# Kernel tuning notes

Hardware: AMD Instinct MI355X
Metric: run time of the kernel (lower is better)

Reference implementation:

```python
import jax, jax.numpy as jnp
import numpy as np

TS = 1.0  # simulation time step (Ts from network.yaml)


def alpha_psp(x, tau):
    """SLAYER psp: causal temporal conv of x (time-major, (T,...)) with the
    SRM alpha kernel eps[k] = (k*Ts/tau)*exp(1 - k*Ts/tau), scaled by Ts.
    eps[k] = (Ts*e/tau) * k * d**k with d = exp(-Ts/tau), realized exactly by a
    2-state linear recurrence instead of an O(T^2) FIR."""
    d = jnp.asarray(np.exp(-TS / tau), x.dtype)
    c = jnp.asarray(np.e * TS / tau * TS, x.dtype)  # kernel amp * Ts integration

    def step(carry, x_t):
        u, v = carry                       # u = sum x_s d^(t-1-s); v = sum x_s (t-1-s) d^(t-1-s)
        v_new = d * (v + u)                # -> sum_{s<=t} x_s (t-s) d^(t-s)  (x_t weight 0)
        u_new = d * u + x_t
        return (u_new, v_new), c * v_new

    z = jnp.zeros_like(x[0])
    _, out = jax.lax.scan(step, (z, z), x)
    return out


def lif_spike(u_in, theta, tauRef, scaleRef):
    """SLAYER spike function: sequential threshold over time with alpha-shaped
    refractory response nu[k] = -scaleRef*theta*(k*Ts/tauRef)*exp(1-k*Ts/tauRef)
    added after every spike. Same 2-state recurrence generates the refractory
    sum exactly. u_in is time-major (T, ...). Spike amplitude is 1/Ts."""
    d = jnp.asarray(np.exp(-TS / tauRef), u_in.dtype)
    c = jnp.asarray(-scaleRef * theta * np.e * TS / tauRef, u_in.dtype)

    def step(carry, u_t):
        u, v = carry
        v_new = d * (v + u)                # refractory state from past spikes only
        m = u_t + c * v_new                # membrane potential incl. refractory
        s = (m >= theta).astype(u_t.dtype)
        return (d * u + s, v_new), (s / TS, m)

    z = jnp.zeros_like(u_in[0])
    _, (spikes, membrane) = jax.lax.scan(step, (z, z), u_in)
    return spikes, membrane


def conv2d_t(x, w, pad):
    """Per-time-step 2D conv (SLAYER conv3d with time-kernel 1, no bias).
    x: (T, N, C, H, W), w: (O, I, kh, kw)."""
    T, N, C, H, W = x.shape
    y = jax.lax.conv_general_dilated(
        x.reshape(T * N, C, H, W), w, (1, 1), [(pad, pad), (pad, pad)],
        dimension_numbers=('NCHW', 'OIHW', 'NCHW'))
    return y.reshape(T, N, -1, H, W)


def setup_inputs() -> dict:
    key = jax.random.key(0)
    k1, k2, k3 = jax.random.split(key, 3)
    # binary event spike train, (N, C, H, W, T)
    spikeInput = (jax.random.uniform(k1, (4, 1, 192, 192, 64)) < 0.2).astype(jnp.float32)
    # SLAYER conv weights (bias=False); scaled up (weightScale~100 in SLAYER)
    W1 = jax.random.normal(k2, (1, 1, 5, 5), jnp.float32) * 10.0
    W2 = jax.random.normal(k3, (1, 1, 3, 3), jnp.float32) * 10.0
    return {"spikeInput": spikeInput, "W1": W1, "W2": W2}


def reference(spikeInput, W1, W2):
    x = jnp.moveaxis(spikeInput, -1, 0)          # (T, N, C, H, W) time-major
    psp1 = alpha_psp(x, tau=1.0)                 # slayer1.psp (tauSr=1)
    s1, _ = lif_spike(conv2d_t(psp1, W1, 2), theta=30.0, tauRef=1.0, scaleRef=1.0)
    psp2 = alpha_psp(s1, tau=2.0)                # slayer2.psp (tauSr=2)
    s2, _ = lif_spike(conv2d_t(psp2, W2, 1), theta=50.0, tauRef=2.0, scaleRef=1.0)
    return jnp.moveaxis(s2, 0, -1)               # back to (N, C, H, W, T)
```

## Files before the change

kernel.cpp:

```cpp
#include <hip/hip_runtime.h>


#define HH   192
#define WW   192
#define NIMG 4
#define TT   64
#define NT   256
#define XW   6
#define XH   12

#define E_D 2.718281828459045
static constexpr float D1  = (float)0.36787944117144233;
static constexpr float CP1 = (float)(E_D);
static constexpr float DR1 = (float)0.36787944117144233;
static constexpr float CR1 = (float)(-30.0 * E_D);
static constexpr float D2  = (float)0.6065306597126334;
static constexpr float CP2 = (float)(E_D * 0.5);
static constexpr float DR2 = (float)0.6065306597126334;
static constexpr float CR2 = (float)(-50.0 * E_D * 0.5);
static constexpr float TH1 = 30.0f;
static constexpr float TH2 = 50.0f;

__global__ __launch_bounds__(NT)
void ka_pack(const float* __restrict__ in, unsigned* __restrict__ bitT) {
    const int gw = blockIdx.x * (NT / 64) + (threadIdx.x >> 6);
    const int ln = threadIdx.x & 63;
    const int xw = gw % XW;
    const int ny = gw / XW;
    const float* src = in + ((size_t)ny * WW + xw * 32) * TT + ln;
    unsigned w = 0u;
#pragma unroll
    for (int x = 0; x < 32; x++) {
        const float v = src[(size_t)x * TT];
        w |= (v != 0.f) ? (1u << x) : 0u;
    }
    bitT[((size_t)ny * XW + xw) * TT + ln] = w;
}

__global__ __launch_bounds__(NT, 1)
void kb_layer1(const unsigned* __restrict__ bitT, const float* __restrict__ w1g,
               unsigned short* __restrict__ s1h) {
    __shared__ float lutA[1024];
    __shared__ float lutB[1024];
    __shared__ float lutC[32];
    __shared__ float ct[NT * 65];
    __shared__ uint2 tb[NT];

    const int n = blockIdx.z, ty = blockIdx.y, tx = blockIdx.x;
    const int y0 = ty * 16, x0 = tx * 16;
    const int tid = threadIdx.x;
    const int wv = tid >> 6, ln = tid & 63;

    for (int e = tid; e < 1024; e += NT) {
        float l0 = 0.f, l1 = 0.f, l2 = 0.f, l3 = 0.f;
#pragma unroll
        for (int j = 0; j < 5; j++) {
            if ((e >> j) & 1)       { l0 += w1g[j];     l2 += w1g[10 + j]; }
            if ((e >> (5 + j)) & 1) { l1 += w1g[5 + j]; l3 += w1g[15 + j]; }
        }
        lutA[e] = l0 + l1;
        lutB[e] = l2 + l3;
    }
    if (tid < 32) {
        float s = 0.f;
#pragma unroll
        for (int j = 0; j < 5; j++)
            if ((tid >> j) & 1) s += w1g[20 + j];
        lutC[tid] = s;
    }

    const int a = (x0 - 2) >> 5;
    const int s = (x0 - 2) & 31;
    unsigned w20[8];
#pragma unroll
    for (int rr = 0; rr < 8; rr++) {
        const int gy = y0 - 2 + wv * 4 + rr;
        unsigned wa = 0u, wb = 0u;
        if (gy >= 0 && gy < HH) {
            const unsigned* rp = bitT + ((size_t)(n * HH + gy) * XW) * TT + ln;
            if (a >= 0)     wa = rp[(size_t)a * TT];
            if (a + 1 < XW) wb = rp[(size_t)(a + 1) * TT];
        }
        w20[rr] = (wa >> s) | (wb << (32 - s));
    }
    __syncthreads();

#pragma unroll
    for (int rp = 0; rp < 4; rp++) {
        const int row = wv * 4 + rp;
#pragma unroll
        for (int col = 0; col < 16; col++) {
            const unsigned pA = ((w20[rp + 0] >> col) & 31)
                              | (((w20[rp + 1] >> col) & 31) << 5);
            const unsigned pB = ((w20[rp + 2] >> col) & 31)
                              | (((w20[rp + 3] >> col) & 31) << 5);
            const unsigned pC = (w20[rp + 4] >> col) & 31;
            ct[(row * 16 + col) * 65 + ln] = (lutA[pA] + lutB[pB]) + lutC[pC];
        }
    }
    __syncthreads();

    unsigned slo = 0u, shi = 0u;
    {
        const int px = tid;
        float u1 = 0.f, v1 = 0.f, ur = 0.f, vr = 0.f;
#pragma unroll
        for (int tc = 0; tc < TT; tc += 8) {
            float c8[8];
#pragma unroll
            for (int j = 0; j < 8; j++) c8[j] = ct[px * 65 + tc + j];
#pragma unroll
            for (int j = 0; j < 8; j++) {
                v1 = D1 * (v1 + u1);
                const float p = CP1 * v1;
                u1 = D1 * u1 + c8[j];
                vr = DR1 * (vr + ur);
                const float m = p + CR1 * vr;
                const bool sp = (m >= TH1);
                ur = DR1 * ur + (sp ? 1.f : 0.f);
                const unsigned bit = sp ? (1u << ((tc + j) & 31)) : 0u;
                if (tc < 32) slo |= bit;
                else         shi |= bit;
            }
        }
    }
    tb[tid] = make_uint2(slo, shi);
    __syncthreads();

#pragma unroll
    for (int rp = 0; rp < 4; rp++) {
        const int yl = wv * 4 + rp;
        unsigned h = 0u;
#pragma unroll
        for (int x = 0; x < 16; x++) {
            const uint2 b = tb[yl * 16 + x];
            const unsigned w = (ln < 32) ? b.x : b.y;
            h |= ((w >> (ln & 31)) & 1u) << x;
        }
        s1h[((size_t)(n * HH + y0 + yl) * XH + tx) * TT + ln] =
            (unsigned short)h;
    }
}

__global__ __launch_bounds__(NT, 1)
void kc_layer2(const unsigned short* __restrict__ s1h, const float* __restrict__ w2g,
               float* __restrict__ out) {
    __shared__ float lut3[512];
    __shared__ unsigned short ptile[NT * 66];
    __shared__ uint2 tb[NT];

    const int n = blockIdx.z, ty = blockIdx.y, tx = blockIdx.x;
    const int y0 = ty * 16;
    const int tid = threadIdx.x;
    const int wv = tid >> 6, ln = tid & 63;

#pragma unroll
    for (int e = tid; e < 512; e += NT) {
        float l0 = 0.f, l1 = 0.f, l2 = 0.f;
#pragma unroll
        for (int j = 0; j < 3; j++) {
            if ((e >> j) & 1)       l0 += w2g[j];
            if ((e >> (3 + j)) & 1) l1 += w2g[3 + j];
            if ((e >> (6 + j)) & 1) l2 += w2g[6 + j];
        }
        lut3[e] = (l0 + l1) + l2;
    }

    unsigned w18[6];
#pragma unroll
    for (int rr = 0; rr < 6; rr++) {
        const int gy = y0 - 1 + wv * 4 + rr;
        unsigned hm = 0u, h0 = 0u, hp = 0u;
        if (gy >= 0 && gy < HH) {
            const unsigned short* rp = s1h + ((size_t)(n * HH + gy) * XH) * TT + ln;
            if (tx > 0)      hm = rp[(size_t)(tx - 1) * TT];
            h0 = rp[(size_t)tx * TT];
            if (tx + 1 < XH) hp = rp[(size_t)(tx + 1) * TT];
        }
        w18[rr] = (hm >> 15) | (h0 << 1) | ((hp & 1u) << 17);
    }
    __syncthreads();

#pragma unroll
    for (int rp = 0; rp < 4; rp++) {
        const int row = wv * 4 + rp;
#pragma unroll
        for (int col = 0; col < 16; col++) {
            const unsigned pat = ((w18[rp + 0] >> col) & 7)
                               | (((w18[rp + 1] >> col) & 7) << 3)
                               | (((w18[rp + 2] >> col) & 7) << 6);
            ptile[(row * 16 + col) * 66 + ln] = (unsigned short)pat;
        }
    }
    __syncthreads();

    unsigned olo = 0u, ohi = 0u;
    {
        const int px = tid;
        const unsigned* pp = (const unsigned*)(ptile + px * 66);
        float u2 = 0.f, v2 = 0.f, ur2 = 0.f, vr2 = 0.f;
#pragma unroll
        for (int tc = 0; tc < TT; tc += 8) {
            unsigned q[4];
#pragma unroll
            for (int k = 0; k < 4; k++) q[k] = pp[tc / 2 + k];
            float l[8];
#pragma unroll
            for (int k = 0; k < 4; k++) {
                l[2 * k + 0] = lut3[q[k] & 0x1ffu];
                l[2 * k + 1] = lut3[(q[k] >> 16) & 0x1ffu];
            }
#pragma unroll
            for (int j = 0; j < 8; j++) {
                v2 = D2 * (v2 + u2);
                const float p = CP2 * v2;
                u2 = D2 * u2 + l[j];
                vr2 = DR2 * (vr2 + ur2);
                const float m = p + CR2 * vr2;
                const bool sp = (m >= TH2);
                ur2 = DR2 * ur2 + (sp ? 1.f : 0.f);
                const unsigned bit = sp ? (1u << ((tc + j) & 31)) : 0u;
                if (tc < 32) olo |= bit;
                else         ohi |= bit;
            }
        }
    }
    tb[tid] = make_uint2(olo, ohi);
    __syncthreads();

    const int sh = ln & 31;
#pragma unroll
    for (int k = 0; k < 64; k++) {
        const int p = wv * 64 + k;
        const uint2 b = tb[p];
        const unsigned w = (ln < 32) ? b.x : b.y;
        out[((size_t)(n * HH + y0 + (p >> 4)) * WW + tx * 16 + (p & 15)) * TT
            + ln] = (float)((w >> sh) & 1u);
    }
}

extern "C" void kernel_launch(void* const* d_in, const int* in_sizes, int n_in,
                              void* d_out, int out_size, void* d_ws, size_t ws_size,
                              hipStream_t stream) {
    const float* in = (const float*)d_in[0];
    const float* w1 = (const float*)d_in[1];
    const float* w2 = (const float*)d_in[2];
    float* out = (float*)d_out;

    char* ws = (char*)d_ws;
    unsigned*       bitT = (unsigned*)ws;
    unsigned short* s1h  = (unsigned short*)(ws + (2ull << 20));

    const int ka_blocks = (NIMG * HH * XW) / (NT / 64);
    dim3 tgrid(WW / 16, HH / 16, NIMG);
    ka_pack  <<<ka_blocks, NT, 0, stream>>>(in, bitT);
    kb_layer1<<<tgrid, NT, 0, stream>>>(bitT, w1, s1h);
    kc_layer2<<<tgrid, NT, 0, stream>>>(s1h, w2, out);
}
```

Before: 123.7 us.

## Fuse input bit-packing into layer1 kernel and widen blocks to 1024 threads

Removes the separate packing kernel. Layer1 now reads the float input directly and builds 20-bit row masks, including the halo, into shared memory. Both tile kernels move to 1024-thread blocks, with one wave per output row for the pattern and output stages, while only 256 threads run the sequential time recurrence. This saves a launch and the bitT round trip through global memory. In exchange, halo columns are read redundantly from the float input, and most threads sit idle during the serial recurrence.

```diff
diff --git a/kernel.cpp b/kernel.cpp
--- a/kernel.cpp
+++ b/kernel.cpp
@@ -5,8 +5,7 @@
 #define WW   192
 #define NIMG 4
 #define TT   64
-#define NT   256
-#define XW   6
+#define NT   1024
 #define XH   12
 
 #define E_D 2.718281828459045
@@ -21,37 +20,23 @@
 static constexpr float TH1 = 30.0f;
 static constexpr float TH2 = 50.0f;
 
-__global__ __launch_bounds__(NT)
-void ka_pack(const float* __restrict__ in, unsigned* __restrict__ bitT) {
-    const int gw = blockIdx.x * (NT / 64) + (threadIdx.x >> 6);
-    const int ln = threadIdx.x & 63;
-    const int xw = gw % XW;
-    const int ny = gw / XW;
-    const float* src = in + ((size_t)ny * WW + xw * 32) * TT + ln;
-    unsigned w = 0u;
-#pragma unroll
-    for (int x = 0; x < 32; x++) {
-        const float v = src[(size_t)x * TT];
-        w |= (v != 0.f) ? (1u << x) : 0u;
-    }
-    bitT[((size_t)ny * XW + xw) * TT + ln] = w;
-}
-
 __global__ __launch_bounds__(NT, 1)
-void kb_layer1(const unsigned* __restrict__ bitT, const float* __restrict__ w1g,
+void kb_layer1(const float* __restrict__ in, const float* __restrict__ w1g,
                unsigned short* __restrict__ s1h) {
-    __shared__ float lutA[1024];
-    __shared__ float lutB[1024];
-    __shared__ float lutC[32];
-    __shared__ float ct[NT * 65];
-    __shared__ uint2 tb[NT];
+    __shared__ float    lutA[1024];
+    __shared__ float    lutB[1024];
+    __shared__ float    lutC[32];
+    __shared__ unsigned rowT[20 * 64];
+    __shared__ float    ct[256 * 65];
+    __shared__ uint2    tb[256];
 
     const int n = blockIdx.z, ty = blockIdx.y, tx = blockIdx.x;
     const int y0 = ty * 16, x0 = tx * 16;
     const int tid = threadIdx.x;
     const int wv = tid >> 6, ln = tid & 63;
 
-    for (int e = tid; e < 1024; e += NT) {
+    {
+        const int e = tid;
         float l0 = 0.f, l1 = 0.f, l2 = 0.f, l3 = 0.f;
 #pragma unroll
         for (int j = 0; j < 5; j++) {
@@ -69,41 +54,44 @@
         lutC[tid] = s;
     }
 
-    const int a = (x0 - 2) >> 5;
-    const int s = (x0 - 2) & 31;
-    unsigned w20[8];
-#pragma unroll
-    for (int rr = 0; rr < 8; rr++) {
-        const int gy = y0 - 2 + wv * 4 + rr;
-        unsigned wa = 0u, wb = 0u;
+    for (int r = wv; r < 20; r += 16) {
+        const int gy = y0 - 2 + r;
+        unsigned word = 0u;
         if (gy >= 0 && gy < HH) {
-            const unsigned* rp = bitT + ((size_t)(n * HH + gy) * XW) * TT + ln;
-            if (a >= 0)     wa = rp[(size_t)a * TT];
-            if (a + 1 < XW) wb = rp[(size_t)(a + 1) * TT];
-        }
-        w20[rr] = (wa >> s) | (wb << (32 - s));
-    }
-    __syncthreads();
-
-#pragma unroll
-    for (int rp = 0; rp < 4; rp++) {
-        const int row = wv * 4 + rp;
+            const float* rowp = in + ((size_t)(n * HH + gy) * WW) * TT + ln;
+#pragma unroll
+            for (int c = 0; c < 20; c++) {
+                const int gx = x0 - 2 + c;
+                if (gx >= 0 && gx < WW) {
+                    const float v = rowp[(size_t)gx * TT];
+                    word |= (v != 0.f) ? (1u << c) : 0u;
+                }
+            }
+        }
+        rowT[r * 64 + ln] = word;
+    }
+    __syncthreads();
+
+    {
+        unsigned w20[5];
+#pragma unroll
+        for (int dy = 0; dy < 5; dy++) w20[dy] = rowT[(wv + dy) * 64 + ln];
 #pragma unroll
         for (int col = 0; col < 16; col++) {
-            const unsigned pA = ((w20[rp + 0] >> col) & 31)
-                              | (((w20[rp + 1] >> col) & 31) << 5);
-            const unsigned pB = ((w20[rp + 2] >> col) & 31)
-                              | (((w20[rp + 3] >> col) & 31) << 5);
-            const unsigned pC = (w20[rp + 4] >> col) & 31;
-            ct[(row * 16 + col) * 65 + ln] = (lutA[pA] + lutB[pB]) + lutC[pC];
-        }
-    }
-    __syncthreads();
-
-    unsigned slo = 0u, shi = 0u;
-    {
+            const unsigned pA = ((w20[0] >> col) & 31)
+                              | (((w20[1] >> col) & 31) << 5);
+            const unsigned pB = ((w20[2] >> col) & 31)
+                              | (((w20[3] >> col) & 31) << 5);
+            const unsigned pC = (w20[4] >> col) & 31;
+            ct[(wv * 16 + col) * 65 + ln] = (lutA[pA] + lutB[pB]) + lutC[pC];
+        }
+    }
+    __syncthreads();
+
+    if (tid < 256) {
         const int px = tid;
         float u1 = 0.f, v1 = 0.f, ur = 0.f, vr = 0.f;
+        unsigned slo = 0u, shi = 0u;
 #pragma unroll
         for (int tc = 0; tc < TT; tc += 8) {
             float c8[8];
@@ -123,21 +111,19 @@
                 else         shi |= bit;
             }
         }
-    }
-    tb[tid] = make_uint2(slo, shi);
-    __syncthreads();
-
-#pragma unroll
-    for (int rp = 0; rp < 4; rp++) {
-        const int yl = wv * 4 + rp;
+        tb[px] = make_uint2(slo, shi);
+    }
+    __syncthreads();
+
+    {
         unsigned h = 0u;
 #pragma unroll
         for (int x = 0; x < 16; x++) {
-            const uint2 b = tb[yl * 16 + x];
+            const uint2 b = tb[wv * 16 + x];
             const unsigned w = (ln < 32) ? b.x : b.y;
             h |= ((w >> (ln & 31)) & 1u) << x;
         }
-        s1h[((size_t)(n * HH + y0 + yl) * XH + tx) * TT + ln] =
+        s1h[((size_t)(n * HH + y0 + wv) * XH + tx) * TT + ln] =
             (unsigned short)h;
     }
 }
@@ -145,17 +131,18 @@
 __global__ __launch_bounds__(NT, 1)
 void kc_layer2(const unsigned short* __restrict__ s1h, const float* __restrict__ w2g,
                float* __restrict__ out) {
-    __shared__ float lut3[512];
-    __shared__ unsigned short ptile[NT * 66];
-    __shared__ uint2 tb[NT];
+    __shared__ float          lut3[512];
+    __shared__ unsigned       wrow[18 * 64];
+    __shared__ unsigned short ptile[256 * 66];
+    __shared__ uint2          tb[256];
 
     const int n = blockIdx.z, ty = blockIdx.y, tx = blockIdx.x;
     const int y0 = ty * 16;
     const int tid = threadIdx.x;
     const int wv = tid >> 6, ln = tid & 63;
 
-#pragma unroll
-    for (int e = tid; e < 512; e += NT) {
+    if (tid < 512) {
+        const int e = tid;
         float l0 = 0.f, l1 = 0.f, l2 = 0.f;
 #pragma unroll
         for (int j = 0; j < 3; j++) {
@@ -166,39 +153,39 @@
         lut3[e] = (l0 + l1) + l2;
     }
 
-    unsigned w18[6];
-#pragma unroll
-    for (int rr = 0; rr < 6; rr++) {
-        const int gy = y0 - 1 + wv * 4 + rr;
+    for (int r = wv; r < 18; r += 16) {
+        const int gy = y0 - 1 + r;
         unsigned hm = 0u, h0 = 0u, hp = 0u;
         if (gy >= 0 && gy < HH) {
-            const unsigned short* rp = s1h + ((size_t)(n * HH + gy) * XH) * TT + ln;
+            const unsigned short* rp =
+                s1h + ((size_t)(n * HH + gy) * XH) * TT + ln;
             if (tx > 0)      hm = rp[(size_t)(tx - 1) * TT];
             h0 = rp[(size_t)tx * TT];
             if (tx + 1 < XH) hp = rp[(size_t)(tx + 1) * TT];
         }
-        w18[rr] = (hm >> 15) | (h0 << 1) | ((hp & 1u) << 17);
-    }
-    __syncthreads();
-
-#pragma unroll
-    for (int rp = 0; rp < 4; rp++) {
-        const int row = wv * 4 + rp;
+        wrow[r * 64 + ln] = (hm >> 15) | (h0 << 1) | ((hp & 1u) << 17);
+    }
+    __syncthreads();
+
+    {
+        unsigned w18[3];
+#pragma unroll
+        for (int dy = 0; dy < 3; dy++) w18[dy] = wrow[(wv + dy) * 64 + ln];
 #pragma unroll
         for (int col = 0; col < 16; col++) {
-            const unsigned pat = ((w18[rp + 0] >> col) & 7)
-                               | (((w18[rp + 1] >> col) & 7) << 3)
-                               | (((w18[rp + 2] >> col) & 7) << 6);
-            ptile[(row * 16 + col) * 66 + ln] = (unsigned short)pat;
-        }
-    }
-    __syncthreads();
-
-    unsigned olo = 0u, ohi = 0u;
-    {
+            const unsigned pat = ((w18[0] >> col) & 7)
+                               | (((w18[1] >> col) & 7) << 3)
+                               | (((w18[2] >> col) & 7) << 6);
+            ptile[(wv * 16 + col) * 66 + ln] = (unsigned short)pat;
+        }
+    }
+    __syncthreads();
+
+    if (tid < 256) {
         const int px = tid;
         const unsigned* pp = (const unsigned*)(ptile + px * 66);
         float u2 = 0.f, v2 = 0.f, ur2 = 0.f, vr2 = 0.f;
+        unsigned olo = 0u, ohi = 0u;
 #pragma unroll
         for (int tc = 0; tc < TT; tc += 8) {
             unsigned q[4];
@@ -224,18 +211,17 @@
                 else         ohi |= bit;
             }
         }
-    }
-    tb[tid] = make_uint2(olo, ohi);
+        tb[px] = make_uint2(olo, ohi);
+    }
     __syncthreads();
 
     const int sh = ln & 31;
 #pragma unroll
-    for (int k = 0; k < 64; k++) {
-        const int p = wv * 64 + k;
-        const uint2 b = tb[p];
+    for (int k = 0; k < 16; k++) {
+        const uint2 b = tb[wv * 16 + k];
         const unsigned w = (ln < 32) ? b.x : b.y;
-        out[((size_t)(n * HH + y0 + (p >> 4)) * WW + tx * 16 + (p & 15)) * TT
-            + ln] = (float)((w >> sh) & 1u);
+        out[((size_t)(n * HH + y0 + wv) * WW + tx * 16 + k) * TT + ln] =
+            (float)((w >> sh) & 1u);
     }
 }
 
@@ -247,13 +233,9 @@
     const float* w2 = (const float*)d_in[2];
     float* out = (float*)d_out;
 
-    char* ws = (char*)d_ws;
-    unsigned*       bitT = (unsigned*)ws;
-    unsigned short* s1h  = (unsigned short*)(ws + (2ull << 20));
-
-    const int ka_blocks = (NIMG * HH * XW) / (NT / 64);
+    unsigned short* s1h = (unsigned short*)d_ws;
+
     dim3 tgrid(WW / 16, HH / 16, NIMG);
-    ka_pack  <<<ka_blocks, NT, 0, stream>>>(in, bitT);
-    kb_layer1<<<tgrid, NT, 0, stream>>>(bitT, w1, s1h);
+    kb_layer1<<<tgrid, NT, 0, stream>>>(in, w1, s1h);
     kc_layer2<<<tgrid, NT, 0, stream>>>(s1h, w2, out);
 }
```

Result: slower. 148.4 us (+19.9%).

## Shrink conv-scan tiles to 4x16 pixels with one scan wave per block

Applied to the files above, without the earlier changes.

Both layer kernels now process a 4-row by 16-column tile per block instead of 16x16, giving four times as many blocks, and each block's LDS shrinks enough for several to fit per CU. Only the first wave runs the sequential time scan (64 pixels), while all four waves build the conv tile and write outputs. The aim is more blocks and more concurrent waves to hide the latency of the serial scan and of the global loads. The cost is three of four waves idling during the scan, and LUT construction plus halo row loads being repeated across four times as many blocks.

```diff
diff --git a/kernel.cpp b/kernel.cpp
--- a/kernel.cpp
+++ b/kernel.cpp
@@ -37,20 +37,21 @@
     bitT[((size_t)ny * XW + xw) * TT + ln] = w;
 }
 
-__global__ __launch_bounds__(NT, 1)
-void kb_layer1(const unsigned* __restrict__ bitT, const float* __restrict__ w1g,
-               unsigned short* __restrict__ s1h) {
+__global__ __launch_bounds__(NT, 4)
+void l1_convscan(const unsigned* __restrict__ bitT, const float* __restrict__ w1g,
+                 unsigned short* __restrict__ s1h) {
     __shared__ float lutA[1024];
     __shared__ float lutB[1024];
     __shared__ float lutC[32];
-    __shared__ float ct[NT * 65];
-    __shared__ uint2 tb[NT];
-
-    const int n = blockIdx.z, ty = blockIdx.y, tx = blockIdx.x;
-    const int y0 = ty * 16, x0 = tx * 16;
+    __shared__ float ct[64 * 65];
+    __shared__ uint2 tb[64];
+
+    const int n = blockIdx.z, ys = blockIdx.y, xs = blockIdx.x;
+    const int y0 = ys * 4, x0 = xs * 16;
     const int tid = threadIdx.x;
     const int wv = tid >> 6, ln = tid & 63;
 
+#pragma unroll
     for (int e = tid; e < 1024; e += NT) {
         float l0 = 0.f, l1 = 0.f, l2 = 0.f, l3 = 0.f;
 #pragma unroll
@@ -71,39 +72,34 @@
 
     const int a = (x0 - 2) >> 5;
     const int s = (x0 - 2) & 31;
-    unsigned w20[8];
-#pragma unroll
-    for (int rr = 0; rr < 8; rr++) {
-        const int gy = y0 - 2 + wv * 4 + rr;
+    const int gyb = y0 + wv;
+    unsigned w20[5];
+#pragma unroll
+    for (int dy = 0; dy < 5; dy++) {
+        const int gy = gyb - 2 + dy;
         unsigned wa = 0u, wb = 0u;
         if (gy >= 0 && gy < HH) {
             const unsigned* rp = bitT + ((size_t)(n * HH + gy) * XW) * TT + ln;
             if (a >= 0)     wa = rp[(size_t)a * TT];
             if (a + 1 < XW) wb = rp[(size_t)(a + 1) * TT];
         }
-        w20[rr] = (wa >> s) | (wb << (32 - s));
-    }
-    __syncthreads();
-
-#pragma unroll
-    for (int rp = 0; rp < 4; rp++) {
-        const int row = wv * 4 + rp;
-#pragma unroll
-        for (int col = 0; col < 16; col++) {
-            const unsigned pA = ((w20[rp + 0] >> col) & 31)
-                              | (((w20[rp + 1] >> col) & 31) << 5);
-            const unsigned pB = ((w20[rp + 2] >> col) & 31)
-                              | (((w20[rp + 3] >> col) & 31) << 5);
-            const unsigned pC = (w20[rp + 4] >> col) & 31;
-            ct[(row * 16 + col) * 65 + ln] = (lutA[pA] + lutB[pB]) + lutC[pC];
-        }
-    }
-    __syncthreads();
-
-    unsigned slo = 0u, shi = 0u;
-    {
+        w20[dy] = (wa >> s) | (wb << (32 - s));
+    }
+    __syncthreads();
+
+#pragma unroll
+    for (int col = 0; col < 16; col++) {
+        const unsigned pA = ((w20[0] >> col) & 31) | (((w20[1] >> col) & 31) << 5);
+        const unsigned pB = ((w20[2] >> col) & 31) | (((w20[3] >> col) & 31) << 5);
+        const unsigned pC = (w20[4] >> col) & 31;
+        ct[(wv * 16 + col) * 65 + ln] = (lutA[pA] + lutB[pB]) + lutC[pC];
+    }
+    __syncthreads();
+
+    if (tid < 64) {
         const int px = tid;
         float u1 = 0.f, v1 = 0.f, ur = 0.f, vr = 0.f;
+        unsigned slo = 0u, shi = 0u;
 #pragma unroll
         for (int tc = 0; tc < TT; tc += 8) {
             float c8[8];
@@ -123,34 +119,31 @@
                 else         shi |= bit;
             }
         }
-    }
-    tb[tid] = make_uint2(slo, shi);
-    __syncthreads();
-
-#pragma unroll
-    for (int rp = 0; rp < 4; rp++) {
-        const int yl = wv * 4 + rp;
+        tb[px] = make_uint2(slo, shi);
+    }
+    __syncthreads();
+
+    {
         unsigned h = 0u;
 #pragma unroll
         for (int x = 0; x < 16; x++) {
-            const uint2 b = tb[yl * 16 + x];
+            const uint2 b = tb[wv * 16 + x];
             const unsigned w = (ln < 32) ? b.x : b.y;
             h |= ((w >> (ln & 31)) & 1u) << x;
         }
-        s1h[((size_t)(n * HH + y0 + yl) * XH + tx) * TT + ln] =
-            (unsigned short)h;
-    }
-}
-
-__global__ __launch_bounds__(NT, 1)
-void kc_layer2(const unsigned short* __restrict__ s1h, const float* __restrict__ w2g,
-               float* __restrict__ out) {
-    __shared__ float lut3[512];
-    __shared__ unsigned short ptile[NT * 66];
-    __shared__ uint2 tb[NT];
-
-    const int n = blockIdx.z, ty = blockIdx.y, tx = blockIdx.x;
-    const int y0 = ty * 16;
+        s1h[((size_t)(n * HH + gyb) * XH + xs) * TT + ln] = (unsigned short)h;
+    }
+}
+
+__global__ __launch_bounds__(NT, 4)
+void l2_convscan(const unsigned short* __restrict__ s1h, const float* __restrict__ w2g,
+                 float* __restrict__ out) {
+    __shared__ float          lut3[512];
+    __shared__ unsigned short ptile[64 * 66];
+    __shared__ uint2          tb[64];
+
+    const int n = blockIdx.z, ys = blockIdx.y, xs = blockIdx.x;
+    const int y0 = ys * 4;
     const int tid = threadIdx.x;
     const int wv = tid >> 6, ln = tid & 63;
 
@@ -166,39 +159,36 @@
         lut3[e] = (l0 + l1) + l2;
     }
 
-    unsigned w18[6];
-#pragma unroll
-    for (int rr = 0; rr < 6; rr++) {
-        const int gy = y0 - 1 + wv * 4 + rr;
+    const int gyb = y0 + wv;
+    unsigned w18[3];
+#pragma unroll
+    for (int dy = 0; dy < 3; dy++) {
+        const int gy = gyb - 1 + dy;
         unsigned hm = 0u, h0 = 0u, hp = 0u;
         if (gy >= 0 && gy < HH) {
             const unsigned short* rp = s1h + ((size_t)(n * HH + gy) * XH) * TT + ln;
-            if (tx > 0)      hm = rp[(size_t)(tx - 1) * TT];
-            h0 = rp[(size_t)tx * TT];
-            if (tx + 1 < XH) hp = rp[(size_t)(tx + 1) * TT];
-        }
-        w18[rr] = (hm >> 15) | (h0 << 1) | ((hp & 1u) << 17);
-    }
-    __syncthreads();
-
-#pragma unroll
-    for (int rp = 0; rp < 4; rp++) {
-        const int row = wv * 4 + rp;
-#pragma unroll
-        for (int col = 0; col < 16; col++) {
-            const unsigned pat = ((w18[rp + 0] >> col) & 7)
-                               | (((w18[rp + 1] >> col) & 7) << 3)
-                               | (((w18[rp + 2] >> col) & 7) << 6);
-            ptile[(row * 16 + col) * 66 + ln] = (unsigned short)pat;
-        }
-    }
-    __syncthreads();
-
-    unsigned olo = 0u, ohi = 0u;
-    {
+            if (xs > 0)      hm = rp[(size_t)(xs - 1) * TT];
+            h0 = rp[(size_t)xs * TT];
+            if (xs + 1 < XH) hp = rp[(size_t)(xs + 1) * TT];
+        }
+        w18[dy] = (hm >> 15) | (h0 << 1) | ((hp & 1u) << 17);
+    }
+    __syncthreads();
+
+#pragma unroll
+    for (int col = 0; col < 16; col++) {
+        const unsigned pat = ((w18[0] >> col) & 7)
+                           | (((w18[1] >> col) & 7) << 3)
+                           | (((w18[2] >> col) & 7) << 6);
+        ptile[(wv * 16 + col) * 66 + ln] = (unsigned short)pat;
+    }
+    __syncthreads();
+
+    if (tid < 64) {
         const int px = tid;
         const unsigned* pp = (const unsigned*)(ptile + px * 66);
         float u2 = 0.f, v2 = 0.f, ur2 = 0.f, vr2 = 0.f;
+        unsigned olo = 0u, ohi = 0u;
 #pragma unroll
         for (int tc = 0; tc < TT; tc += 8) {
             unsigned q[4];
@@ -224,18 +214,17 @@
                 else         ohi |= bit;
             }
         }
-    }
-    tb[tid] = make_uint2(olo, ohi);
+        tb[px] = make_uint2(olo, ohi);
+    }
     __syncthreads();
 
     const int sh = ln & 31;
 #pragma unroll
-    for (int k = 0; k < 64; k++) {
-        const int p = wv * 64 + k;
-        const uint2 b = tb[p];
+    for (int k = 0; k < 16; k++) {
+        const uint2 b = tb[wv * 16 + k];
         const unsigned w = (ln < 32) ? b.x : b.y;
-        out[((size_t)(n * HH + y0 + (p >> 4)) * WW + tx * 16 + (p & 15)) * TT
-            + ln] = (float)((w >> sh) & 1u);
+        out[((size_t)(n * HH + gyb) * WW + xs * 16 + k) * TT + ln] =
+            (float)((w >> sh) & 1u);
     }
 }
 
@@ -252,8 +241,8 @@
     unsigned short* s1h  = (unsigned short*)(ws + (2ull << 20));
 
     const int ka_blocks = (NIMG * HH * XW) / (NT / 64);
-    dim3 tgrid(WW / 16, HH / 16, NIMG);
-    ka_pack  <<<ka_blocks, NT, 0, stream>>>(in, bitT);
-    kb_layer1<<<tgrid, NT, 0, stream>>>(bitT, w1, s1h);
-    kc_layer2<<<tgrid, NT, 0, stream>>>(s1h, w2, out);
-}
+    dim3 cgrid(WW / 16, HH / 4, NIMG);
+    ka_pack    <<<ka_blocks, NT, 0, stream>>>(in, bitT);
+    l1_convscan<<<cgrid, NT, 0, stream>>>(bitT, w1, s1h);
+    l2_convscan<<<cgrid, NT, 0, stream>>>(s1h, w2, out);
+}
```

New measurement: 119.0 us. 1.04x faster.
